# Performance work log

Measured on AMD Instinct MI355X. Metric: run time of the kernel, lower is better.

The kernel has to match this reference:

```python
import jax, jax.numpy as jnp
import numpy as np

B, C, LX, LY, H = 8, 128, 4096, 1024, 4
DH = C // H


def setup_inputs() -> dict:
    key = jax.random.key(0)
    ks = jax.random.split(key, 12)
    s = 0.05
    return {
        "x": jax.random.normal(ks[0], (B, C, LX), jnp.float32),
        "y": jax.random.normal(ks[1], (B, C, LY), jnp.float32),
        # nn.MultiheadAttention combined in-projection [3C, C] and bias [3C]
        "in_proj_w": jax.random.normal(ks[2], (3 * C, C), jnp.float32) * s,
        "in_proj_b": jax.random.normal(ks[3], (3 * C,), jnp.float32) * s,
        # local_att: Conv1d(C,32,1) then Conv1d(32,1,1); kernel_size=1 -> stored as matrices
        "conv1_w": jax.random.normal(ks[4], (32, C), jnp.float32) * s,
        "conv1_b": jax.random.normal(ks[5], (32,), jnp.float32) * s,
        "conv2_w": jax.random.normal(ks[6], (1, 32), jnp.float32) * s,
        "conv2_b": jax.random.normal(ks[7], (1,), jnp.float32) * s,
        # gate_mlp: Linear(2, 1)
        "gate_w": jax.random.normal(ks[8], (1, 2), jnp.float32) * s,
        "gate_b": jax.random.normal(ks[9], (1,), jnp.float32) * s,
    }


def reference(x, y, in_proj_w, in_proj_b, conv1_w, conv1_b, conv2_w, conv2_b, gate_w, gate_b):
    # x: [B,C,Lx] (query side), y: [B,C,Ly] (key/value side)
    wq, wk = in_proj_w[:C], in_proj_w[C:2 * C]
    bq, bk = in_proj_b[:C], in_proj_b[C:2 * C]

    xt = jnp.swapaxes(x, 1, 2)  # [B,Lx,C]
    yt = jnp.swapaxes(y, 1, 2)  # [B,Ly,C]

    q = (xt @ wq.T + bq).reshape(B, LX, H, DH)
    k = (yt @ wk.T + bk).reshape(B, LY, H, DH)

    scores = jnp.einsum('bqhd,bkhd->bhqk', q, k) / jnp.sqrt(jnp.float32(DH))  # [B,H,Lx,Ly]
    attn = jax.nn.softmax(scores, axis=-1)
    # torch MHA returns head-averaged weights (average_attn_weights=True)
    cross_weights = attn.mean(axis=1)            # [B,Lx,Ly]
    cross_scores = cross_weights.max(axis=-1)    # [B,Lx]
    # (attn_output / V / out_proj are unused downstream in the original forward)

    # local conv scoring (1x1 convs == channel matmuls)
    h = jax.nn.relu(jnp.einsum('oc,bcl->bol', conv1_w, x) + conv1_b[None, :, None])
    local_scores = jax.nn.sigmoid(jnp.einsum('po,bol->bpl', conv2_w, h) + conv2_b[None, :, None])[:, 0, :]  # [B,Lx]

    gating = jnp.stack((cross_scores, local_scores), axis=-1)  # [B,Lx,2]
    alpha = jax.nn.sigmoid(gating @ gate_w.T + gate_b)[..., 0]  # [B,Lx]
    return alpha * cross_scores + (1.0 - alpha) * local_scores
```

## Files before the change

### kernel.cpp

```cpp
#include <hip/hip_runtime.h>
#include <hip/hip_bf16.h>

#define BB  8
#define CC  128
#define LXX 4096
#define LYY 1024
#define HH  4
#define DHH 32

typedef __attribute__((ext_vector_type(8))) short bf16x8;
typedef __attribute__((ext_vector_type(4))) float f32x4;

static __device__ __forceinline__ unsigned short f2bf(float f) {
    __hip_bfloat16 h = __float2bfloat16(f);
    return *reinterpret_cast<unsigned short*>(&h);
}

static __device__ __forceinline__ bf16x8 pack8(const float* f) {
    bf16x8 r;
#pragma unroll
    for (int i = 0; i < 8; ++i) {
        __hip_bfloat16 h = __float2bfloat16(f[i]);
        r[i] = *reinterpret_cast<short*>(&h);
    }
    return r;
}

static __device__ __forceinline__ bf16x8 ldw8(const float* p) {
    float t[8];
    *(float4*)(t)     = *(const float4*)(p);
    *(float4*)(t + 4) = *(const float4*)(p + 4);
    return pack8(t);
}

__global__ __launch_bounds__(256) void kproj_pre_kernel(
    const float* __restrict__ y, const float* __restrict__ ipw,
    const float* __restrict__ ipb, const float* __restrict__ c1w,
    unsigned short* __restrict__ Kb, unsigned short* __restrict__ wbf)
{
    int tid  = threadIdx.x;
    int blk  = blockIdx.x;

    if (blk >= 256) {
        int base = (blk - 256) * 2304;
#pragma unroll
        for (int j = 0; j < 9; ++j) {
            int idx = base + j * 256 + tid;
            float v = (idx < 2 * CC * CC) ? ipw[idx] : c1w[idx - 2 * CC * CC];
            wbf[idx] = f2bf(v);
        }
        return;
    }

    int wv   = tid >> 6;
    int lane = tid & 63;
    int n16  = lane & 15;
    int quad = lane >> 4;

    int bi = blk >> 5;
    int rest = blk & 31;
    int l0 = (rest >> 1) * 64;
    int mh = rest & 1;
    const float* src  = y + (size_t)bi * CC * LYY;
    const float* wrow = ipw + CC * CC;
    const float* bias = ipb + CC;
    int myl = l0 + wv * 16 + n16;

    bf16x8 bfr[4];
#pragma unroll
    for (int kk = 0; kk < 4; ++kk) {
        float t[8];
        const float* p = src + (size_t)(kk * 32 + quad * 8) * LYY + myl;
#pragma unroll
        for (int j = 0; j < 8; ++j) t[j] = p[(size_t)j * LYY];
        bfr[kk] = pack8(t);
    }

    const f32x4 fzero = {0.f, 0.f, 0.f, 0.f};
#pragma unroll 1
    for (int mi = 0; mi < 4; ++mi) {
        int m = mh * 4 + mi;
        int mc = m * 16;
        f32x4 acc = fzero;
#pragma unroll
        for (int kk = 0; kk < 4; ++kk)
            acc = __builtin_amdgcn_mfma_f32_16x16x32_bf16(
                ldw8(wrow + (size_t)(mc + n16) * CC + kk * 32 + quad * 8),
                bfr[kk], acc, 0, 0, 0);
        int h = mc >> 5, d0 = (mc & 31) + quad * 4;
        float4 bq = *(const float4*)(bias + mc + quad * 4);
        ushort4 u;
        u.x = f2bf(acc[0] + bq.x);
        u.y = f2bf(acc[1] + bq.y);
        u.z = f2bf(acc[2] + bq.z);
        u.w = f2bf(acc[3] + bq.w);
        *(ushort4*)(Kb + (((size_t)(bi * HH + h) * LYY) + myl) * DHH + d0) = u;
    }
}

__global__ __launch_bounds__(256, 4) void attn_fused_kernel(
    const float* __restrict__ x, const unsigned short* __restrict__ Kh,
    const unsigned short* __restrict__ wbf, const float* __restrict__ ipb,
    const float* __restrict__ c1b,
    const float* __restrict__ c2w, const float* __restrict__ c2b,
    const float* __restrict__ gw, const float* __restrict__ gb,
    float* __restrict__ out, float qscale)
{
    int tid = threadIdx.x;
    int w = tid >> 6;
    int lane = tid & 63;
    int n16 = lane & 15;
    int quad = lane >> 4;
    int bi = blockIdx.y;
    int q0 = blockIdx.x * 32;

    __shared__ float xls[32][132];
    __shared__ unsigned short qlds[2][16][136];
    __shared__ float dlds[4][2][HH][16];
    __shared__ float mlds[4][2][16];
    __shared__ float plds[32];

    const float* xsrc = x + (size_t)bi * CC * LXX;
    const unsigned short* wc1 = wbf + 2 * CC * CC;
    const f32x4 fzero = {0.f, 0.f, 0.f, 0.f};

#pragma unroll
    for (int i = 0; i < 4; ++i) {
        int idx = i * 256 + tid;
        int c  = idx >> 3;
        int l4 = (idx & 7) * 4;
        float4 v = *(const float4*)(xsrc + (size_t)c * LXX + q0 + l4);
        xls[l4 + 0][c] = v.x;
        xls[l4 + 1][c] = v.y;
        xls[l4 + 2][c] = v.z;
        xls[l4 + 3][c] = v.w;
    }
    bf16x8 wf[2][4];
#pragma unroll
    for (int mi = 0; mi < 2; ++mi)
#pragma unroll
        for (int kk = 0; kk < 4; ++kk)
            wf[mi][kk] = *(const bf16x8*)(wbf +
                (size_t)((2 * w + mi) * 16 + n16) * CC + kk * 32 + quad * 8);
    __syncthreads();

    bf16x8 bq[2][4];
#pragma unroll
    for (int qt = 0; qt < 2; ++qt)
#pragma unroll
        for (int kk = 0; kk < 4; ++kk) {
            float t[8];
            *(float4*)(t)     = *(const float4*)(&xls[qt * 16 + n16][kk * 32 + quad * 8]);
            *(float4*)(t + 4) = *(const float4*)(&xls[qt * 16 + n16][kk * 32 + quad * 8 + 4]);
            bq[qt][kk] = pack8(t);
        }

#pragma unroll
    for (int qt = 0; qt < 2; ++qt) {
#pragma unroll
        for (int mi = 0; mi < 2; ++mi) {
            int m = 2 * w + mi;
            f32x4 acc = fzero;
#pragma unroll
            for (int kk = 0; kk < 4; ++kk)
                acc = __builtin_amdgcn_mfma_f32_16x16x32_bf16(wf[mi][kk], bq[qt][kk], acc, 0, 0, 0);
            float4 bv = *(const float4*)(ipb + m * 16 + quad * 4);
            ushort4 u;
            u.x = f2bf((acc[0] + bv.x) * qscale);
            u.y = f2bf((acc[1] + bv.y) * qscale);
            u.z = f2bf((acc[2] + bv.z) * qscale);
            u.w = f2bf((acc[3] + bv.w) * qscale);
            *(ushort4*)(&qlds[qt][n16][m * 16 + quad * 4]) = u;
        }
        if (w == 2 + qt) {
            float p = 0.f;
#pragma unroll
            for (int m2 = 0; m2 < 2; ++m2) {
                f32x4 hacc = fzero;
#pragma unroll
                for (int kk = 0; kk < 4; ++kk)
                    hacc = __builtin_amdgcn_mfma_f32_16x16x32_bf16(
                        *(const bf16x8*)(wc1 + (size_t)(m2 * 16 + n16) * CC + kk * 32 + quad * 8),
                        bq[qt][kk], hacc, 0, 0, 0);
#pragma unroll
                for (int r = 0; r < 4; ++r) {
                    int o = m2 * 16 + quad * 4 + r;
                    p = fmaf(c2w[o], fmaxf(hacc[r] + c1b[o], 0.0f), p);
                }
            }
            p += __shfl_xor(p, 16, 64);
            p += __shfl_xor(p, 32, 64);
            if (quad == 0)
                plds[qt * 16 + n16] = 1.0f / (1.0f + __expf(-(p + c2b[0])));
        }
    }
    __syncthreads();

    bf16x8 afr[2][HH];
#pragma unroll
    for (int qt = 0; qt < 2; ++qt)
#pragma unroll
        for (int h = 0; h < HH; ++h)
            afr[qt][h] = *(const bf16x8*)(&qlds[qt][n16][h * 32 + quad * 8]);

    const unsigned short* Kbase = Kh + (((size_t)bi * HH) * LYY + w * 256 + n16) * DHH + quad * 8;

    f32x4 den[2][HH];
#pragma unroll
    for (int qt = 0; qt < 2; ++qt)
#pragma unroll
        for (int h = 0; h < HH; ++h) den[qt][h] = fzero;

#pragma unroll 2
    for (int t = 0; t < 16; ++t) {
        bf16x8 bfr[HH];
#pragma unroll
        for (int h = 0; h < HH; ++h)
            bfr[h] = *(const bf16x8*)(Kbase + ((size_t)h * LYY + t * 16) * DHH);
#pragma unroll
        for (int h = 0; h < HH; ++h) {
            f32x4 s0 = __builtin_amdgcn_mfma_f32_16x16x32_bf16(afr[0][h], bfr[h], fzero, 0, 0, 0);
            f32x4 s1 = __builtin_amdgcn_mfma_f32_16x16x32_bf16(afr[1][h], bfr[h], fzero, 0, 0, 0);
#pragma unroll
            for (int r = 0; r < 4; ++r) {
                den[0][h][r] += __builtin_amdgcn_exp2f(s0[r]);
                den[1][h][r] += __builtin_amdgcn_exp2f(s1[r]);
            }
        }
    }
#pragma unroll
    for (int off = 1; off < 16; off <<= 1)
#pragma unroll
        for (int qt = 0; qt < 2; ++qt)
#pragma unroll
            for (int h = 0; h < HH; ++h)
#pragma unroll
                for (int r = 0; r < 4; ++r)
                    den[qt][h][r] += __shfl_xor(den[qt][h][r], off, 64);
    if (n16 == 0) {
#pragma unroll
        for (int qt = 0; qt < 2; ++qt)
#pragma unroll
            for (int h = 0; h < HH; ++h)
#pragma unroll
                for (int r = 0; r < 4; ++r) dlds[w][qt][h][quad * 4 + r] = den[qt][h][r];
    }
    __syncthreads();

    f32x4 cc[2][HH];
#pragma unroll
    for (int qt = 0; qt < 2; ++qt)
#pragma unroll
        for (int h = 0; h < HH; ++h)
#pragma unroll
            for (int r = 0; r < 4; ++r) {
                int row = quad * 4 + r;
                float d = dlds[0][qt][h][row] + dlds[1][qt][h][row] +
                          dlds[2][qt][h][row] + dlds[3][qt][h][row];
                cc[qt][h][r] = -__builtin_amdgcn_logf(d);
            }

    f32x4 vm0 = fzero, vm1 = fzero;
#pragma unroll 2
    for (int t = 0; t < 16; ++t) {
        bf16x8 bfr[HH];
#pragma unroll
        for (int h = 0; h < HH; ++h)
            bfr[h] = *(const bf16x8*)(Kbase + ((size_t)h * LYY + t * 16) * DHH);
        f32x4 f0 = fzero, f1 = fzero;
#pragma unroll
        for (int h = 0; h < HH; ++h) {
            f32x4 s0 = __builtin_amdgcn_mfma_f32_16x16x32_bf16(afr[0][h], bfr[h], cc[0][h], 0, 0, 0);
            f32x4 s1 = __builtin_amdgcn_mfma_f32_16x16x32_bf16(afr[1][h], bfr[h], cc[1][h], 0, 0, 0);
#pragma unroll
            for (int r = 0; r < 4; ++r) {
                f0[r] += __builtin_amdgcn_exp2f(s0[r]);
                f1[r] += __builtin_amdgcn_exp2f(s1[r]);
            }
        }
#pragma unroll
        for (int r = 0; r < 4; ++r) {
            vm0[r] = fmaxf(vm0[r], f0[r]);
            vm1[r] = fmaxf(vm1[r], f1[r]);
        }
    }
#pragma unroll
    for (int off = 1; off < 16; off <<= 1)
#pragma unroll
        for (int r = 0; r < 4; ++r) {
            vm0[r] = fmaxf(vm0[r], __shfl_xor(vm0[r], off, 64));
            vm1[r] = fmaxf(vm1[r], __shfl_xor(vm1[r], off, 64));
        }
    if (n16 == 0) {
#pragma unroll
        for (int r = 0; r < 4; ++r) {
            mlds[w][0][quad * 4 + r] = vm0[r];
            mlds[w][1][quad * 4 + r] = vm1[r];
        }
    }
    __syncthreads();
    if (tid < 32) {
        int qq = tid >> 4;
        int row = tid & 15;
        float m = fmaxf(fmaxf(mlds[0][qq][row], mlds[1][qq][row]),
                        fmaxf(mlds[2][qq][row], mlds[3][qq][row]));
        float cs = 0.25f * m;
        int orow = q0 + qq * 16 + row;
        float ls = plds[qq * 16 + row];
        float z = gw[0] * cs + gw[1] * ls + gb[0];
        float alpha = 1.0f / (1.0f + __expf(-z));
        out[(size_t)bi * LXX + orow] = alpha * cs + (1.0f - alpha) * ls;
    }
}

extern "C" void kernel_launch(void* const* d_in, const int* in_sizes, int n_in,
                              void* d_out, int out_size, void* d_ws, size_t ws_size,
                              hipStream_t stream) {
    const float* x   = (const float*)d_in[0];
    const float* y   = (const float*)d_in[1];
    const float* ipw = (const float*)d_in[2];
    const float* ipb = (const float*)d_in[3];
    const float* c1w = (const float*)d_in[4];
    const float* c1b = (const float*)d_in[5];
    const float* c2w = (const float*)d_in[6];
    const float* c2b = (const float*)d_in[7];
    const float* gw  = (const float*)d_in[8];
    const float* gb  = (const float*)d_in[9];
    float* out = (float*)d_out;

    unsigned short* Kb  = (unsigned short*)d_ws;
    unsigned short* wbf = Kb + (size_t)BB * HH * LYY * DHH;

    const float qscale = 0.17677669529663687f * 1.4426950408889634f;

    hipLaunchKernelGGL(kproj_pre_kernel, dim3(272), dim3(256), 0, stream,
                       y, ipw, ipb, c1w, Kb, wbf);
    hipLaunchKernelGGL(attn_fused_kernel, dim3(LXX / 32, BB), dim3(256), 0, stream,
                       x, Kb, wbf, ipb, c1b, c2w, c2b, gw, gb, out, qscale);
}
```

Before: 128.8 us.

## Fuse K projection into attention kernel with global atomic grid barrier

```diff
diff --git a/kernel.cpp b/kernel.cpp
--- a/kernel.cpp
+++ b/kernel.cpp
@@ -33,77 +33,13 @@
     return pack8(t);
 }
 
-__global__ __launch_bounds__(256) void kproj_pre_kernel(
-    const float* __restrict__ y, const float* __restrict__ ipw,
-    const float* __restrict__ ipb, const float* __restrict__ c1w,
-    unsigned short* __restrict__ Kb, unsigned short* __restrict__ wbf)
-{
-    int tid  = threadIdx.x;
-    int blk  = blockIdx.x;
-
-    if (blk >= 256) {
-        int base = (blk - 256) * 2304;
-#pragma unroll
-        for (int j = 0; j < 9; ++j) {
-            int idx = base + j * 256 + tid;
-            float v = (idx < 2 * CC * CC) ? ipw[idx] : c1w[idx - 2 * CC * CC];
-            wbf[idx] = f2bf(v);
-        }
-        return;
-    }
-
-    int wv   = tid >> 6;
-    int lane = tid & 63;
-    int n16  = lane & 15;
-    int quad = lane >> 4;
-
-    int bi = blk >> 5;
-    int rest = blk & 31;
-    int l0 = (rest >> 1) * 64;
-    int mh = rest & 1;
-    const float* src  = y + (size_t)bi * CC * LYY;
-    const float* wrow = ipw + CC * CC;
-    const float* bias = ipb + CC;
-    int myl = l0 + wv * 16 + n16;
-
-    bf16x8 bfr[4];
-#pragma unroll
-    for (int kk = 0; kk < 4; ++kk) {
-        float t[8];
-        const float* p = src + (size_t)(kk * 32 + quad * 8) * LYY + myl;
-#pragma unroll
-        for (int j = 0; j < 8; ++j) t[j] = p[(size_t)j * LYY];
-        bfr[kk] = pack8(t);
-    }
-
-    const f32x4 fzero = {0.f, 0.f, 0.f, 0.f};
-#pragma unroll 1
-    for (int mi = 0; mi < 4; ++mi) {
-        int m = mh * 4 + mi;
-        int mc = m * 16;
-        f32x4 acc = fzero;
-#pragma unroll
-        for (int kk = 0; kk < 4; ++kk)
-            acc = __builtin_amdgcn_mfma_f32_16x16x32_bf16(
-                ldw8(wrow + (size_t)(mc + n16) * CC + kk * 32 + quad * 8),
-                bfr[kk], acc, 0, 0, 0);
-        int h = mc >> 5, d0 = (mc & 31) + quad * 4;
-        float4 bq = *(const float4*)(bias + mc + quad * 4);
-        ushort4 u;
-        u.x = f2bf(acc[0] + bq.x);
-        u.y = f2bf(acc[1] + bq.y);
-        u.z = f2bf(acc[2] + bq.z);
-        u.w = f2bf(acc[3] + bq.w);
-        *(ushort4*)(Kb + (((size_t)(bi * HH + h) * LYY) + myl) * DHH + d0) = u;
-    }
-}
-
-__global__ __launch_bounds__(256, 4) void attn_fused_kernel(
-    const float* __restrict__ x, const unsigned short* __restrict__ Kh,
-    const unsigned short* __restrict__ wbf, const float* __restrict__ ipb,
-    const float* __restrict__ c1b,
+__global__ __launch_bounds__(256, 4) void fused_all_kernel(
+    const float* __restrict__ x, const float* __restrict__ y,
+    const float* __restrict__ ipw, const float* __restrict__ ipb,
+    const float* __restrict__ c1w, const float* __restrict__ c1b,
     const float* __restrict__ c2w, const float* __restrict__ c2b,
     const float* __restrict__ gw, const float* __restrict__ gb,
+    unsigned short* __restrict__ Kb, unsigned int* __restrict__ done,
     float* __restrict__ out, float qscale)
 {
     int tid = threadIdx.x;
@@ -113,6 +49,7 @@
     int quad = lane >> 4;
     int bi = blockIdx.y;
     int q0 = blockIdx.x * 32;
+    int fb = bi * 128 + blockIdx.x;
 
     __shared__ float xls[32][132];
     __shared__ unsigned short qlds[2][16][136];
@@ -120,10 +57,48 @@
     __shared__ float mlds[4][2][16];
     __shared__ float plds[32];
 
+    const f32x4 fzero = {0.f, 0.f, 0.f, 0.f};
+
+    {
+        int bik = fb >> 7;
+        int l0k = ((fb >> 3) & 15) * 64;
+        int m   = fb & 7;
+        const float* srcK  = y + (size_t)bik * CC * LYY;
+        const float* wrow  = ipw + CC * CC;
+        const float* biasK = ipb + CC;
+        int mylK = l0k + w * 16 + n16;
+
+        bf16x8 bfrK[4];
+#pragma unroll
+        for (int kk = 0; kk < 4; ++kk) {
+            float t[8];
+            const float* p = srcK + (size_t)(kk * 32 + quad * 8) * LYY + mylK;
+#pragma unroll
+            for (int j = 0; j < 8; ++j) t[j] = p[(size_t)j * LYY];
+            bfrK[kk] = pack8(t);
+        }
+        int mc = m * 16;
+        f32x4 acc = fzero;
+#pragma unroll
+        for (int kk = 0; kk < 4; ++kk)
+            acc = __builtin_amdgcn_mfma_f32_16x16x32_bf16(
+                ldw8(wrow + (size_t)(mc + n16) * CC + kk * 32 + quad * 8),
+                bfrK[kk], acc, 0, 0, 0);
+        int h = mc >> 5, d0 = (mc & 31) + quad * 4;
+        float4 bq4 = *(const float4*)(biasK + mc + quad * 4);
+        ushort4 u;
+        u.x = f2bf(acc[0] + bq4.x);
+        u.y = f2bf(acc[1] + bq4.y);
+        u.z = f2bf(acc[2] + bq4.z);
+        u.w = f2bf(acc[3] + bq4.w);
+        *(ushort4*)(Kb + (((size_t)(bik * HH + h) * LYY) + mylK) * DHH + d0) = u;
+    }
+
+    __syncthreads();
+    if (tid == 0)
+        __hip_atomic_fetch_add(done, 1u, __ATOMIC_RELEASE, __HIP_MEMORY_SCOPE_AGENT);
+
     const float* xsrc = x + (size_t)bi * CC * LXX;
-    const unsigned short* wc1 = wbf + 2 * CC * CC;
-    const f32x4 fzero = {0.f, 0.f, 0.f, 0.f};
-
 #pragma unroll
     for (int i = 0; i < 4; ++i) {
         int idx = i * 256 + tid;
@@ -140,8 +115,7 @@
     for (int mi = 0; mi < 2; ++mi)
 #pragma unroll
         for (int kk = 0; kk < 4; ++kk)
-            wf[mi][kk] = *(const bf16x8*)(wbf +
-                (size_t)((2 * w + mi) * 16 + n16) * CC + kk * 32 + quad * 8);
+            wf[mi][kk] = ldw8(ipw + (size_t)((2 * w + mi) * 16 + n16) * CC + kk * 32 + quad * 8);
     __syncthreads();
 
     bf16x8 bq[2][4];
@@ -180,7 +154,7 @@
 #pragma unroll
                 for (int kk = 0; kk < 4; ++kk)
                     hacc = __builtin_amdgcn_mfma_f32_16x16x32_bf16(
-                        *(const bf16x8*)(wc1 + (size_t)(m2 * 16 + n16) * CC + kk * 32 + quad * 8),
+                        ldw8(c1w + (size_t)(m2 * 16 + n16) * CC + kk * 32 + quad * 8),
                         bq[qt][kk], hacc, 0, 0, 0);
 #pragma unroll
                 for (int r = 0; r < 4; ++r) {
@@ -203,7 +177,13 @@
         for (int h = 0; h < HH; ++h)
             afr[qt][h] = *(const bf16x8*)(&qlds[qt][n16][h * 32 + quad * 8]);
 
-    const unsigned short* Kbase = Kh + (((size_t)bi * HH) * LYY + w * 256 + n16) * DHH + quad * 8;
+    if (tid == 0) {
+        while (__hip_atomic_load(done, __ATOMIC_ACQUIRE, __HIP_MEMORY_SCOPE_AGENT) < 1024u)
+            __builtin_amdgcn_s_sleep(8);
+    }
+    __syncthreads();
+
+    const unsigned short* Kbase = Kb + (((size_t)bi * HH) * LYY + w * 256 + n16) * DHH + quad * 8;
 
     f32x4 den[2][HH];
 #pragma unroll
@@ -328,13 +308,14 @@
     const float* gb  = (const float*)d_in[9];
     float* out = (float*)d_out;
 
-    unsigned short* Kb  = (unsigned short*)d_ws;
-    unsigned short* wbf = Kb + (size_t)BB * HH * LYY * DHH;
+    unsigned short* Kb = (unsigned short*)d_ws;
+    unsigned int* done = (unsigned int*)(Kb + (size_t)BB * HH * LYY * DHH);
+
+    hipMemsetAsync(done, 0, sizeof(unsigned int), stream);
 
     const float qscale = 0.17677669529663687f * 1.4426950408889634f;
 
-    hipLaunchKernelGGL(kproj_pre_kernel, dim3(272), dim3(256), 0, stream,
-                       y, ipw, ipb, c1w, Kb, wbf);
-    hipLaunchKernelGGL(attn_fused_kernel, dim3(LXX / 32, BB), dim3(256), 0, stream,
-                       x, Kb, wbf, ipb, c1b, c2w, c2b, gw, gb, out, qscale);
-}
+    hipLaunchKernelGGL(fused_all_kernel, dim3(LXX / 32, BB), dim3(256), 0, stream,
+                       x, y, ipw, ipb, c1w, c1b, c2w, c2b, gw, gb,
+                       Kb, done, out, qscale);
+}
```

New measurement: 170.8 us. 32.7% more time.
